# Kernel tuning notes

Hardware: AMD Instinct MI355X
Metric: run time of the kernel (lower is better)

Reference implementation:

```python
import jax, jax.numpy as jnp
import numpy as np

PATCH = 14   # vision_config.patch_size
MERGE = 2    # spatial_merge_size
D = 1024     # vision_config.hidden_size
# pixel (H, W) per image; all dims divisible by PATCH*MERGE = 28
IMAGE_SIZES = np.array([[1540, 1232], [1120, 1540], [896, 1260],
                        [1540, 1540], [1260, 896], [728, 1540]], dtype=np.int64)


def setup_inputs() -> dict:
    key = jax.random.key(0)
    k1, k2 = jax.random.split(key)
    hs = IMAGE_SIZES[:, 0] // PATCH
    ws = IMAGE_SIZES[:, 1] // PATCH
    total_tokens = int(np.sum(hs * ws))  # 47820
    image_features = jax.random.normal(k1, (total_tokens, D), dtype=jnp.float32)
    # nn.Linear(D*MERGE**2 -> D, bias=False): weight [D, D*MERGE**2]
    weight = jax.random.normal(k2, (D, D * MERGE * MERGE), dtype=jnp.float32) * 0.02
    return {"image_features": image_features, "weight": weight,
            "image_sizes": IMAGE_SIZES}


def _merge_patches(image_features, image_sizes):
    """Per-image unfold(kernel=stride=MERGE) -> [n_blocks, D*MERGE^2], concatenated."""
    m = MERGE
    d = image_features.shape[-1]
    sizes = np.asarray(image_sizes)
    hs = sizes[:, 0] // PATCH
    ws = sizes[:, 1] // PATCH
    offsets = np.concatenate([[0], np.cumsum(hs * ws)])
    grids = []
    for i in range(sizes.shape[0]):
        h, w = int(hs[i]), int(ws[i])
        x = jax.lax.dynamic_slice_in_dim(image_features, int(offsets[i]), h * w, 0)
        # [h, w, d] -> blocks of m x m; torch unfold layout is (d, kh, kw) channel-major
        x = x.reshape(h // m, m, w // m, m, d)
        x = x.transpose(0, 2, 4, 1, 3)           # [h/m, w/m, d, m, m]
        x = x.reshape((h // m) * (w // m), d * m * m)
        grids.append(x)
    return jnp.concatenate(grids, axis=0)        # [sum(h*w)/m^2, d*m^2]


def reference(image_features, weight, image_sizes):
    merged = _merge_patches(image_features, image_sizes)
    return merged @ weight.T                     # [N_merged, D]
```

## Files before the change

kernel.cpp:

```cpp
#include <hip/hip_runtime.h>
#include <hip/hip_bf16.h>
#include <stdint.h>

#define K_DIM 4096
#define N_DIM 1024
#define M_TOT 11955

#define BM 128
#define BN 128
#define BK 64
#define NWG_M 94
#define NWG 752

__constant__ int c_wm[6]     = {44, 55, 45, 55, 32, 55};
__constant__ int c_w[6]      = {88, 110, 90, 110, 64, 110};
__constant__ int c_tokoff[6] = {0, 9680, 18480, 24240, 36340, 42100};
__constant__ int c_blkoff[6] = {0, 2420, 4620, 6060, 9085, 10525};

typedef __attribute__((ext_vector_type(8))) short bf16x8;
typedef __attribute__((ext_vector_type(4))) float f32x4;

__global__ __launch_bounds__(256) void wperm_cvt(
    const float* __restrict__ src, __hip_bfloat16* __restrict__ dst)
{
    const int n = blockIdx.x >> 1;
    const int t = (blockIdx.x & 1) * 256 + threadIdx.x;
    const float* row = src + (size_t)n * K_DIM + t * 8;
    float4 a = *(const float4*)row;
    float4 b = *(const float4*)(row + 4);
    const float va[8] = {a.x, a.y, a.z, a.w, b.x, b.y, b.z, b.w};
    __hip_bfloat16* drow = dst + (size_t)n * K_DIM + 2 * t;
#pragma unroll
    for (int seg = 0; seg < 4; ++seg) {
        __hip_bfloat162 h = __float22bfloat162_rn(
            make_float2(va[seg], va[4 + seg]));
        *(__hip_bfloat162*)(drow + seg * 1024) = h;
    }
}

__global__ __launch_bounds__(256) void gemm_fused(
    const float* __restrict__ A,
    const __hip_bfloat16* __restrict__ Wp,
    float* __restrict__ C)
{
    __shared__ __align__(16) __hip_bfloat16 lA[BM * BK];
    __shared__ __align__(16) __hip_bfloat16 lB[BN * BK];

    const int f    = blockIdx.x;
    const int xcd  = f & 7;
    const int slot = f >> 3;
    const int gidx = xcd * NWG_M + slot;
    const int mt   = gidx >> 3;
    const int nt   = gidx & 7;
    const int m0 = mt * BM;
    const int n0 = nt * BN;

    const int tid  = threadIdx.x;
    const int lane = tid & 63;
    const int wave = tid >> 6;
    const int wm = (wave >> 1) * 64;
    const int wn = (wave & 1) * 64;
    const int al = lane & 15;
    const int q  = lane >> 4;
    const int al7 = al & 7;

    int t00[4], ww[4];
    const __hip_bfloat16* pBbase[4];
#pragma unroll
    for (int j = 0; j < 4; ++j) {
        const int c = tid + j * 256;
        const int row = c >> 3;
        const int g = (c & 7) ^ (row & 7);
        int gm = m0 + row; if (gm > M_TOT - 1) gm = M_TOT - 1;
        int img = 0;
#pragma unroll
        for (int u = 1; u < 6; ++u) if (gm >= c_blkoff[u]) img = u;
        const int bi = gm - c_blkoff[img];
        const int wmrg = c_wm[img];
        const int gi = bi / wmrg;
        const int gj = bi - gi * wmrg;
        const int w = c_w[img];
        t00[j] = c_tokoff[img] + 2 * gi * w + 2 * gj;
        pBbase[j] = Wp + (size_t)(n0 + row) * K_DIM + g * 8;
        ww[j] = w | (g << 16);
    }

    f32x4 acc[4][4];
#pragma unroll
    for (int i = 0; i < 4; ++i)
#pragma unroll
        for (int j = 0; j < 4; ++j)
            acc[i][j] = (f32x4){0.f, 0.f, 0.f, 0.f};

#pragma unroll
    for (int seg = 0; seg < 4; ++seg) {
        const int kh = seg >> 1, kw = seg & 1;
        const float* pA[4];
        const __hip_bfloat16* pB[4];
#pragma unroll
        for (int j = 0; j < 4; ++j) {
            const int w = ww[j] & 0xffff;
            const int g = ww[j] >> 16;
            pA[j] = A + (size_t)(t00[j] + kh * w + kw) * N_DIM + g * 8;
            pB[j] = pBbase[j] + seg * 1024;
        }
        for (int k2 = 0; k2 < 1024; k2 += BK) {
#pragma unroll
            for (int j = 0; j < 4; ++j)
                __builtin_amdgcn_global_load_lds(
                    (const __attribute__((address_space(1))) void*)(pB[j] + k2),
                    (__attribute__((address_space(3))) void*)(lB + (tid + j * 256) * 8),
                    16, 0, 0);
            float4 ra[4][2];
#pragma unroll
            for (int j = 0; j < 4; ++j) {
                const float4* s = (const float4*)(pA[j] + k2);
                ra[j][0] = s[0];
                ra[j][1] = s[1];
            }
#pragma unroll
            for (int j = 0; j < 4; ++j) {
                union { __hip_bfloat162 h2[4]; uint4 u; } pk;
                pk.h2[0] = __float22bfloat162_rn(make_float2(ra[j][0].x, ra[j][0].y));
                pk.h2[1] = __float22bfloat162_rn(make_float2(ra[j][0].z, ra[j][0].w));
                pk.h2[2] = __float22bfloat162_rn(make_float2(ra[j][1].x, ra[j][1].y));
                pk.h2[3] = __float22bfloat162_rn(make_float2(ra[j][1].z, ra[j][1].w));
                *(uint4*)(lA + (size_t)(tid + j * 256) * 8) = pk.u;
            }
            __syncthreads();

            bf16x8 af[4], bfr[4];
#pragma unroll
            for (int ks = 0; ks < 2; ++ks) {
#pragma unroll
                for (int mi = 0; mi < 4; ++mi) {
                    const int r = wm + mi * 16 + al;
                    const int p = (ks * 4 + q) ^ al7;
                    af[mi] = *(const bf16x8*)(lA + r * BK + p * 8);
                }
#pragma unroll
                for (int ni = 0; ni < 4; ++ni) {
                    const int r = wn + ni * 16 + al;
                    const int p = (ks * 4 + q) ^ al7;
                    bfr[ni] = *(const bf16x8*)(lB + r * BK + p * 8);
                }
#pragma unroll
                for (int mi = 0; mi < 4; ++mi)
#pragma unroll
                    for (int ni = 0; ni < 4; ++ni)
                        acc[mi][ni] = __builtin_amdgcn_mfma_f32_16x16x32_bf16(
                            af[mi], bfr[ni], acc[mi][ni], 0, 0, 0);
            }
            __syncthreads();
        }
    }

#pragma unroll
    for (int mi = 0; mi < 4; ++mi) {
        const int row = m0 + wm + mi * 16 + q * 4;
#pragma unroll
        for (int ni = 0; ni < 4; ++ni) {
            const int col = n0 + wn + ni * 16 + al;
            float* cp = C + (size_t)row * N_DIM + col;
#pragma unroll
            for (int rg = 0; rg < 4; ++rg) {
                if (row + rg < M_TOT) cp[(size_t)rg * N_DIM] = acc[mi][ni][rg];
            }
        }
    }
}

extern "C" void kernel_launch(void* const* d_in, const int* in_sizes, int n_in,
                              void* d_out, int out_size, void* d_ws, size_t ws_size,
                              hipStream_t stream)
{
    const float* feat = (const float*)d_in[0];
    const float* wgt  = (const float*)d_in[1];
    float* out = (float*)d_out;

    __hip_bfloat16* wp = (__hip_bfloat16*)d_ws;

    wperm_cvt<<<2048, 256, 0, stream>>>(wgt, wp);
    gemm_fused<<<NWG, 256, 0, stream>>>(feat, wp, out);
}
```

Measured before the change: 463.9 us.

## Double-buffer LDS tiles to overlap next-tile global loads with MFMA compute

Result: slower. 499.8 us (+7.7%).

```diff
diff --git a/kernel.cpp b/kernel.cpp
--- a/kernel.cpp
+++ b/kernel.cpp
@@ -11,6 +11,7 @@
 #define BK 64
 #define NWG_M 94
 #define NWG 752
+#define KT_TOT 64
 
 __constant__ int c_wm[6]     = {44, 55, 45, 55, 32, 55};
 __constant__ int c_w[6]      = {88, 110, 90, 110, 64, 110};
@@ -43,8 +44,8 @@
     const __hip_bfloat16* __restrict__ Wp,
     float* __restrict__ C)
 {
-    __shared__ __align__(16) __hip_bfloat16 lA[BM * BK];
-    __shared__ __align__(16) __hip_bfloat16 lB[BN * BK];
+    __shared__ __align__(16) __hip_bfloat16 lA[2][BM * BK];
+    __shared__ __align__(16) __hip_bfloat16 lB[2][BN * BK];
 
     const int f    = blockIdx.x;
     const int xcd  = f & 7;
@@ -64,7 +65,7 @@
     const int q  = lane >> 4;
     const int al7 = al & 7;
 
-    int t00[4], ww[4];
+    int t00[4], wwA[4];
     const __hip_bfloat16* pBbase[4];
 #pragma unroll
     for (int j = 0; j < 4; ++j) {
@@ -82,7 +83,46 @@
         const int w = c_w[img];
         t00[j] = c_tokoff[img] + 2 * gi * w + 2 * gj;
         pBbase[j] = Wp + (size_t)(n0 + row) * K_DIM + g * 8;
-        ww[j] = w | (g << 16);
+        wwA[j] = w | (g << 16);
+    }
+
+    auto aptr = [&](int j, int kt) -> const float* {
+        const int seg = kt >> 4;
+        const int k2  = (kt & 15) * BK;
+        const int kh = seg >> 1, kw = seg & 1;
+        const int w = wwA[j] & 0xffff;
+        const int g = wwA[j] >> 16;
+        return A + (size_t)(t00[j] + (kh ? w : 0) + kw) * N_DIM + g * 8 + k2;
+    };
+    auto bptr = [&](int j, int kt) -> const __hip_bfloat16* {
+        const int seg = kt >> 4;
+        const int k2  = (kt & 15) * BK;
+        return pBbase[j] + seg * 1024 + k2;
+    };
+
+    {
+        float4 ra[4][2];
+#pragma unroll
+        for (int j = 0; j < 4; ++j) {
+            const float4* s = (const float4*)aptr(j, 0);
+            ra[j][0] = s[0]; ra[j][1] = s[1];
+        }
+#pragma unroll
+        for (int j = 0; j < 4; ++j)
+            __builtin_amdgcn_global_load_lds(
+                (const __attribute__((address_space(1))) void*)bptr(j, 0),
+                (__attribute__((address_space(3))) void*)(&lB[0][0] + (tid + j * 256) * 8),
+                16, 0, 0);
+#pragma unroll
+        for (int j = 0; j < 4; ++j) {
+            union { __hip_bfloat162 h2[4]; uint4 u; } pk;
+            pk.h2[0] = __float22bfloat162_rn(make_float2(ra[j][0].x, ra[j][0].y));
+            pk.h2[1] = __float22bfloat162_rn(make_float2(ra[j][0].z, ra[j][0].w));
+            pk.h2[2] = __float22bfloat162_rn(make_float2(ra[j][1].x, ra[j][1].y));
+            pk.h2[3] = __float22bfloat162_rn(make_float2(ra[j][1].z, ra[j][1].w));
+            *(uint4*)(&lA[0][0] + (tid + j * 256) * 8) = pk.u;
+        }
+        __syncthreads();
     }
 
     f32x4 acc[4][4];
@@ -92,32 +132,52 @@
         for (int j = 0; j < 4; ++j)
             acc[i][j] = (f32x4){0.f, 0.f, 0.f, 0.f};
 
-#pragma unroll
-    for (int seg = 0; seg < 4; ++seg) {
-        const int kh = seg >> 1, kw = seg & 1;
-        const float* pA[4];
-        const __hip_bfloat16* pB[4];
-#pragma unroll
-        for (int j = 0; j < 4; ++j) {
-            const int w = ww[j] & 0xffff;
-            const int g = ww[j] >> 16;
-            pA[j] = A + (size_t)(t00[j] + kh * w + kw) * N_DIM + g * 8;
-            pB[j] = pBbase[j] + seg * 1024;
-        }
-        for (int k2 = 0; k2 < 1024; k2 += BK) {
+    for (int kt = 0; kt < KT_TOT; ++kt) {
+        const int cur = kt & 1;
+        const int nxt = cur ^ 1;
+        const bool more = (kt + 1 < KT_TOT);
+
+        float4 ra[4][2];
+        if (more) {
+#pragma unroll
+            for (int j = 0; j < 4; ++j) {
+                const float4* s = (const float4*)aptr(j, kt + 1);
+                ra[j][0] = s[0]; ra[j][1] = s[1];
+            }
 #pragma unroll
             for (int j = 0; j < 4; ++j)
                 __builtin_amdgcn_global_load_lds(
-                    (const __attribute__((address_space(1))) void*)(pB[j] + k2),
-                    (__attribute__((address_space(3))) void*)(lB + (tid + j * 256) * 8),
+                    (const __attribute__((address_space(1))) void*)bptr(j, kt + 1),
+                    (__attribute__((address_space(3))) void*)(&lB[nxt][0] + (tid + j * 256) * 8),
                     16, 0, 0);
-            float4 ra[4][2];
-#pragma unroll
-            for (int j = 0; j < 4; ++j) {
-                const float4* s = (const float4*)(pA[j] + k2);
-                ra[j][0] = s[0];
-                ra[j][1] = s[1];
-            }
+        }
+
+        const __hip_bfloat16* la = &lA[cur][0];
+        const __hip_bfloat16* lb = &lB[cur][0];
+        bf16x8 af[4], bfr[4];
+#pragma unroll
+        for (int ks = 0; ks < 2; ++ks) {
+#pragma unroll
+            for (int mi = 0; mi < 4; ++mi) {
+                const int r = wm + mi * 16 + al;
+                const int p = (ks * 4 + q) ^ al7;
+                af[mi] = *(const bf16x8*)(la + r * BK + p * 8);
+            }
+#pragma unroll
+            for (int ni = 0; ni < 4; ++ni) {
+                const int r = wn + ni * 16 + al;
+                const int p = (ks * 4 + q) ^ al7;
+                bfr[ni] = *(const bf16x8*)(lb + r * BK + p * 8);
+            }
+#pragma unroll
+            for (int mi = 0; mi < 4; ++mi)
+#pragma unroll
+                for (int ni = 0; ni < 4; ++ni)
+                    acc[mi][ni] = __builtin_amdgcn_mfma_f32_16x16x32_bf16(
+                        af[mi], bfr[ni], acc[mi][ni], 0, 0, 0);
+        }
+
+        if (more) {
 #pragma unroll
             for (int j = 0; j < 4; ++j) {
                 union { __hip_bfloat162 h2[4]; uint4 u; } pk;
@@ -125,34 +185,10 @@
                 pk.h2[1] = __float22bfloat162_rn(make_float2(ra[j][0].z, ra[j][0].w));
                 pk.h2[2] = __float22bfloat162_rn(make_float2(ra[j][1].x, ra[j][1].y));
                 pk.h2[3] = __float22bfloat162_rn(make_float2(ra[j][1].z, ra[j][1].w));
-                *(uint4*)(lA + (size_t)(tid + j * 256) * 8) = pk.u;
-            }
-            __syncthreads();
-
-            bf16x8 af[4], bfr[4];
-#pragma unroll
-            for (int ks = 0; ks < 2; ++ks) {
-#pragma unroll
-                for (int mi = 0; mi < 4; ++mi) {
-                    const int r = wm + mi * 16 + al;
-                    const int p = (ks * 4 + q) ^ al7;
-                    af[mi] = *(const bf16x8*)(lA + r * BK + p * 8);
-                }
-#pragma unroll
-                for (int ni = 0; ni < 4; ++ni) {
-                    const int r = wn + ni * 16 + al;
-                    const int p = (ks * 4 + q) ^ al7;
-                    bfr[ni] = *(const bf16x8*)(lB + r * BK + p * 8);
-                }
-#pragma unroll
-                for (int mi = 0; mi < 4; ++mi)
-#pragma unroll
-                    for (int ni = 0; ni < 4; ++ni)
-                        acc[mi][ni] = __builtin_amdgcn_mfma_f32_16x16x32_bf16(
-                            af[mi], bfr[ni], acc[mi][ni], 0, 0, 0);
-            }
-            __syncthreads();
-        }
+                *(uint4*)(&lA[nxt][0] + (tid + j * 256) * 8) = pk.u;
+            }
+        }
+        __syncthreads();
     }
 
 #pragma unroll
```

## Pre-unfold activations to bf16 and use double-buffered 256x256 GEMM tiles

Applied to the files above, without the earlier changes.

Result: faster. 448.6 us (-3.3%).

```diff
diff --git a/kernel.cpp b/kernel.cpp
--- a/kernel.cpp
+++ b/kernel.cpp
@@ -6,11 +6,13 @@
 #define N_DIM 1024
 #define M_TOT 11955
 
-#define BM 128
-#define BN 128
+#define BM 256
+#define BN 256
 #define BK 64
-#define NWG_M 94
-#define NWG 752
+#define KT_N 64
+#define M_TILES 47
+#define N_TILES 4
+#define NWG 188
 
 __constant__ int c_wm[6]     = {44, 55, 45, 55, 32, 55};
 __constant__ int c_w[6]      = {88, 110, 90, 110, 64, 110};
@@ -19,6 +21,11 @@
 
 typedef __attribute__((ext_vector_type(8))) short bf16x8;
 typedef __attribute__((ext_vector_type(4))) float f32x4;
+
+#define BARRIER() do { asm volatile("" ::: "memory"); \
+                       __builtin_amdgcn_s_barrier();  \
+                       asm volatile("" ::: "memory"); } while (0)
+#define VMCNT0()  asm volatile("s_waitcnt vmcnt(0)" ::: "memory")
 
 __global__ __launch_bounds__(256) void wperm_cvt(
     const float* __restrict__ src, __hip_bfloat16* __restrict__ dst)
@@ -38,125 +45,164 @@
     }
 }
 
-__global__ __launch_bounds__(256) void gemm_fused(
-    const float* __restrict__ A,
+__global__ __launch_bounds__(256) void unfold_cvt(
+    const float* __restrict__ feat, __hip_bfloat16* __restrict__ Am)
+{
+    const int m = blockIdx.x;
+    const int t = threadIdx.x;
+    const int seg = t >> 6;
+    const int d0 = (t & 63) * 16;
+    int img = 0;
+#pragma unroll
+    for (int u = 1; u < 6; ++u) if (m >= c_blkoff[u]) img = u;
+    const int bi = m - c_blkoff[img];
+    const int wmrg = c_wm[img];
+    const int gi = bi / wmrg;
+    const int gj = bi - gi * wmrg;
+    const int w  = c_w[img];
+    const int kh = seg >> 1, kw = seg & 1;
+    const int tok = c_tokoff[img] + 2 * gi * w + 2 * gj + kh * w + kw;
+    const float4* src = (const float4*)(feat + (size_t)tok * N_DIM + d0);
+    float4 v0 = src[0], v1 = src[1], v2 = src[2], v3 = src[3];
+    union { __hip_bfloat162 h[8]; uint4 u4[2]; } pk;
+    pk.h[0] = __float22bfloat162_rn(make_float2(v0.x, v0.y));
+    pk.h[1] = __float22bfloat162_rn(make_float2(v0.z, v0.w));
+    pk.h[2] = __float22bfloat162_rn(make_float2(v1.x, v1.y));
+    pk.h[3] = __float22bfloat162_rn(make_float2(v1.z, v1.w));
+    pk.h[4] = __float22bfloat162_rn(make_float2(v2.x, v2.y));
+    pk.h[5] = __float22bfloat162_rn(make_float2(v2.z, v2.w));
+    pk.h[6] = __float22bfloat162_rn(make_float2(v3.x, v3.y));
+    pk.h[7] = __float22bfloat162_rn(make_float2(v3.z, v3.w));
+    uint4* dst = (uint4*)(Am + (size_t)m * K_DIM + seg * 1024 + d0);
+    dst[0] = pk.u4[0];
+    dst[1] = pk.u4[1];
+}
+
+__global__ __launch_bounds__(512, 2) void gemm8(
+    const __hip_bfloat16* __restrict__ Am,
     const __hip_bfloat16* __restrict__ Wp,
     float* __restrict__ C)
 {
-    __shared__ __align__(16) __hip_bfloat16 lA[BM * BK];
-    __shared__ __align__(16) __hip_bfloat16 lB[BN * BK];
-
-    const int f    = blockIdx.x;
-    const int xcd  = f & 7;
-    const int slot = f >> 3;
-    const int gidx = xcd * NWG_M + slot;
-    const int mt   = gidx >> 3;
-    const int nt   = gidx & 7;
+    __shared__ __align__(16) __hip_bfloat16 lA[2][BM * BK];
+    __shared__ __align__(16) __hip_bfloat16 lB[2][BN * BK];
+
+    const int orig = blockIdx.x;
+    const int x    = orig & 7;
+    const int idx  = orig >> 3;
+    const int start = (x < 4) ? x * 24 : 96 + (x - 4) * 23;
+    const int wgid  = start + idx;
+    const int mt = wgid >> 2;
+    const int nt = wgid & 3;
     const int m0 = mt * BM;
     const int n0 = nt * BN;
 
     const int tid  = threadIdx.x;
     const int lane = tid & 63;
     const int wave = tid >> 6;
-    const int wm = (wave >> 1) * 64;
-    const int wn = (wave & 1) * 64;
+    const int wm = (wave >> 2) * 128;
+    const int wn = (wave & 3) * 64;
     const int al = lane & 15;
     const int q  = lane >> 4;
     const int al7 = al & 7;
 
-    int t00[4], ww[4];
-    const __hip_bfloat16* pBbase[4];
-#pragma unroll
-    for (int j = 0; j < 4; ++j) {
-        const int c = tid + j * 256;
-        const int row = c >> 3;
-        const int g = (c & 7) ^ (row & 7);
-        int gm = m0 + row; if (gm > M_TOT - 1) gm = M_TOT - 1;
-        int img = 0;
-#pragma unroll
-        for (int u = 1; u < 6; ++u) if (gm >= c_blkoff[u]) img = u;
-        const int bi = gm - c_blkoff[img];
-        const int wmrg = c_wm[img];
-        const int gi = bi / wmrg;
-        const int gj = bi - gi * wmrg;
-        const int w = c_w[img];
-        t00[j] = c_tokoff[img] + 2 * gi * w + 2 * gj;
-        pBbase[j] = Wp + (size_t)(n0 + row) * K_DIM + g * 8;
-        ww[j] = w | (g << 16);
-    }
-
-    f32x4 acc[4][4];
+    const __hip_bfloat16* srcA[4];
+    const __hip_bfloat16* srcB[4];
+#pragma unroll
+    for (int i = 0; i < 4; ++i) {
+        const int c = tid + i * 512;
+        const int r = c >> 3;
+        const int g = (c & 7) ^ (r & 7);
+        int gm = m0 + r; if (gm > M_TOT - 1) gm = M_TOT - 1;
+        srcA[i] = Am + (size_t)gm * K_DIM + g * 8;
+        srcB[i] = Wp + (size_t)(n0 + r) * K_DIM + g * 8;
+    }
+
 #pragma unroll
     for (int i = 0; i < 4; ++i)
+        __builtin_amdgcn_global_load_lds(
+            (const __attribute__((address_space(1))) void*)srcA[i],
+            (__attribute__((address_space(3))) void*)(&lA[0][0] + (tid + i * 512) * 8),
+            16, 0, 0);
+#pragma unroll
+    for (int i = 0; i < 4; ++i)
+        __builtin_amdgcn_global_load_lds(
+            (const __attribute__((address_space(1))) void*)srcB[i],
+            (__attribute__((address_space(3))) void*)(&lB[0][0] + (tid + i * 512) * 8),
+            16, 0, 0);
+    __syncthreads();
+
+    f32x4 acc[8][4];
+#pragma unroll
+    for (int i = 0; i < 8; ++i)
 #pragma unroll
         for (int j = 0; j < 4; ++j)
             acc[i][j] = (f32x4){0.f, 0.f, 0.f, 0.f};
 
-#pragma unroll
-    for (int seg = 0; seg < 4; ++seg) {
-        const int kh = seg >> 1, kw = seg & 1;
-        const float* pA[4];
-        const __hip_bfloat16* pB[4];
-#pragma unroll
-        for (int j = 0; j < 4; ++j) {
-            const int w = ww[j] & 0xffff;
-            const int g = ww[j] >> 16;
-            pA[j] = A + (size_t)(t00[j] + kh * w + kw) * N_DIM + g * 8;
-            pB[j] = pBbase[j] + seg * 1024;
+    for (int kt = 0; kt < KT_N; ++kt) {
+        const int cur = kt & 1;
+        const __hip_bfloat16* la = &lA[cur][0];
+        const __hip_bfloat16* lb = &lB[cur][0];
+        __hip_bfloat16* wa = &lA[cur ^ 1][0];
+        __hip_bfloat16* wb = &lB[cur ^ 1][0];
+        const bool more = (kt + 1 < KT_N);
+        const int koff = (kt + 1) * BK;
+
+        bf16x8 bfr[4][2];
+#pragma unroll
+        for (int p = 0; p < 4; ++p) {
+            if (p == 0) {
+#pragma unroll
+                for (int ks = 0; ks < 2; ++ks)
+#pragma unroll
+                    for (int ni = 0; ni < 4; ++ni) {
+                        const int r = wn + ni * 16 + al;
+                        bfr[ni][ks] = *(const bf16x8*)(
+                            lb + r * BK + (((ks * 4 + q) ^ al7) * 8));
+                    }
+            }
+            bf16x8 af[2][2];
+#pragma unroll
+            for (int ks = 0; ks < 2; ++ks)
+#pragma unroll
+                for (int mm = 0; mm < 2; ++mm) {
+                    const int r = wm + (p * 2 + mm) * 16 + al;
+                    af[mm][ks] = *(const bf16x8*)(
+                        la + r * BK + (((ks * 4 + q) ^ al7) * 8));
+                }
+            if (p == 0 && more) {
+#pragma unroll
+                for (int i = 0; i < 4; ++i)
+                    __builtin_amdgcn_global_load_lds(
+                        (const __attribute__((address_space(1))) void*)(srcA[i] + koff),
+                        (__attribute__((address_space(3))) void*)(wa + (tid + i * 512) * 8),
+                        16, 0, 0);
+            }
+            if (p == 1 && more) {
+#pragma unroll
+                for (int i = 0; i < 4; ++i)
+                    __builtin_amdgcn_global_load_lds(
+                        (const __attribute__((address_space(1))) void*)(srcB[i] + koff),
+                        (__attribute__((address_space(3))) void*)(wb + (tid + i * 512) * 8),
+                        16, 0, 0);
+            }
+            BARRIER();
+            __builtin_amdgcn_s_setprio(1);
+#pragma unroll
+            for (int ks = 0; ks < 2; ++ks)
+#pragma unroll
+                for (int mm = 0; mm < 2; ++mm)
+#pragma unroll
+                    for (int ni = 0; ni < 4; ++ni)
+                        acc[p * 2 + mm][ni] = __builtin_amdgcn_mfma_f32_16x16x32_bf16(
+                            af[mm][ks], bfr[ni][ks], acc[p * 2 + mm][ni], 0, 0, 0);
+            __builtin_amdgcn_s_setprio(0);
+            if (p == 3) VMCNT0();
+            BARRIER();
         }
-        for (int k2 = 0; k2 < 1024; k2 += BK) {
-#pragma unroll
-            for (int j = 0; j < 4; ++j)
-                __builtin_amdgcn_global_load_lds(
-                    (const __attribute__((address_space(1))) void*)(pB[j] + k2),
-                    (__attribute__((address_space(3))) void*)(lB + (tid + j * 256) * 8),
-                    16, 0, 0);
-            float4 ra[4][2];
-#pragma unroll
-            for (int j = 0; j < 4; ++j) {
-                const float4* s = (const float4*)(pA[j] + k2);
-                ra[j][0] = s[0];
-                ra[j][1] = s[1];
-            }
-#pragma unroll
-            for (int j = 0; j < 4; ++j) {
-                union { __hip_bfloat162 h2[4]; uint4 u; } pk;
-                pk.h2[0] = __float22bfloat162_rn(make_float2(ra[j][0].x, ra[j][0].y));
-                pk.h2[1] = __float22bfloat162_rn(make_float2(ra[j][0].z, ra[j][0].w));
-                pk.h2[2] = __float22bfloat162_rn(make_float2(ra[j][1].x, ra[j][1].y));
-                pk.h2[3] = __float22bfloat162_rn(make_float2(ra[j][1].z, ra[j][1].w));
-                *(uint4*)(lA + (size_t)(tid + j * 256) * 8) = pk.u;
-            }
-            __syncthreads();
-
-            bf16x8 af[4], bfr[4];
-#pragma unroll
-            for (int ks = 0; ks < 2; ++ks) {
-#pragma unroll
-                for (int mi = 0; mi < 4; ++mi) {
-                    const int r = wm + mi * 16 + al;
-                    const int p = (ks * 4 + q) ^ al7;
-                    af[mi] = *(const bf16x8*)(lA + r * BK + p * 8);
-                }
-#pragma unroll
-                for (int ni = 0; ni < 4; ++ni) {
-                    const int r = wn + ni * 16 + al;
-                    const int p = (ks * 4 + q) ^ al7;
-                    bfr[ni] = *(const bf16x8*)(lB + r * BK + p * 8);
-                }
-#pragma unroll
-                for (int mi = 0; mi < 4; ++mi)
-#pragma unroll
-                    for (int ni = 0; ni < 4; ++ni)
-                        acc[mi][ni] = __builtin_amdgcn_mfma_f32_16x16x32_bf16(
-                            af[mi], bfr[ni], acc[mi][ni], 0, 0, 0);
-            }
-            __syncthreads();
-        }
-    }
-
-#pragma unroll
-    for (int mi = 0; mi < 4; ++mi) {
+    }
+
+#pragma unroll
+    for (int mi = 0; mi < 8; ++mi) {
         const int row = m0 + wm + mi * 16 + q * 4;
 #pragma unroll
         for (int ni = 0; ni < 4; ++ni) {
@@ -178,8 +224,11 @@
     const float* wgt  = (const float*)d_in[1];
     float* out = (float*)d_out;
 
-    __hip_bfloat16* wp = (__hip_bfloat16*)d_ws;
+    __hip_bfloat16* Am = (__hip_bfloat16*)d_ws;
+    __hip_bfloat16* wp = (__hip_bfloat16*)((char*)d_ws +
+                         (size_t)M_TOT * K_DIM * sizeof(__hip_bfloat16));
 
     wperm_cvt<<<2048, 256, 0, stream>>>(wgt, wp);
-    gemm_fused<<<NWG, 256, 0, stream>>>(feat, wp, out);
-}
+    unfold_cvt<<<M_TOT, 256, 0, stream>>>(feat, Am);
+    gemm8<<<NWG, 512, 0, stream>>>(Am, wp, out);
+}
```

## Split unfold and bf16 conversion into separate pass before GEMM

Applied to the files above, without the earlier changes.

After: 471.0 us. No clear change (+1.5%).

```diff
diff --git a/kernel.cpp b/kernel.cpp
--- a/kernel.cpp
+++ b/kernel.cpp
@@ -38,8 +38,41 @@
     }
 }
 
-__global__ __launch_bounds__(256) void gemm_fused(
-    const float* __restrict__ A,
+__global__ __launch_bounds__(256) void unfold_cvt(
+    const float* __restrict__ feat, __hip_bfloat16* __restrict__ Am)
+{
+    const int m = blockIdx.x;
+    const int t = threadIdx.x;
+    const int seg = t >> 6;
+    const int d0 = (t & 63) * 16;
+    int img = 0;
+#pragma unroll
+    for (int u = 1; u < 6; ++u) if (m >= c_blkoff[u]) img = u;
+    const int bi = m - c_blkoff[img];
+    const int wmrg = c_wm[img];
+    const int gi = bi / wmrg;
+    const int gj = bi - gi * wmrg;
+    const int w  = c_w[img];
+    const int kh = seg >> 1, kw = seg & 1;
+    const int tok = c_tokoff[img] + 2 * gi * w + 2 * gj + kh * w + kw;
+    const float4* src = (const float4*)(feat + (size_t)tok * N_DIM + d0);
+    float4 v0 = src[0], v1 = src[1], v2 = src[2], v3 = src[3];
+    union { __hip_bfloat162 h[8]; uint4 u4[2]; } pk;
+    pk.h[0] = __float22bfloat162_rn(make_float2(v0.x, v0.y));
+    pk.h[1] = __float22bfloat162_rn(make_float2(v0.z, v0.w));
+    pk.h[2] = __float22bfloat162_rn(make_float2(v1.x, v1.y));
+    pk.h[3] = __float22bfloat162_rn(make_float2(v1.z, v1.w));
+    pk.h[4] = __float22bfloat162_rn(make_float2(v2.x, v2.y));
+    pk.h[5] = __float22bfloat162_rn(make_float2(v2.z, v2.w));
+    pk.h[6] = __float22bfloat162_rn(make_float2(v3.x, v3.y));
+    pk.h[7] = __float22bfloat162_rn(make_float2(v3.z, v3.w));
+    uint4* dst = (uint4*)(Am + (size_t)m * K_DIM + seg * 1024 + d0);
+    dst[0] = pk.u4[0];
+    dst[1] = pk.u4[1];
+}
+
+__global__ __launch_bounds__(256) void gemm_bt(
+    const __hip_bfloat16* __restrict__ Am,
     const __hip_bfloat16* __restrict__ Wp,
     float* __restrict__ C)
 {
@@ -49,9 +82,9 @@
     const int f    = blockIdx.x;
     const int xcd  = f & 7;
     const int slot = f >> 3;
-    const int gidx = xcd * NWG_M + slot;
-    const int mt   = gidx >> 3;
-    const int nt   = gidx & 7;
+    const int wgid = xcd * NWG_M + slot;
+    const int mt   = wgid >> 3;
+    const int nt   = wgid & 7;
     const int m0 = mt * BM;
     const int n0 = nt * BN;
 
@@ -64,25 +97,16 @@
     const int q  = lane >> 4;
     const int al7 = al & 7;
 
-    int t00[4], ww[4];
-    const __hip_bfloat16* pBbase[4];
+    const __hip_bfloat16* srcA[4];
+    const __hip_bfloat16* srcB[4];
 #pragma unroll
     for (int j = 0; j < 4; ++j) {
         const int c = tid + j * 256;
         const int row = c >> 3;
         const int g = (c & 7) ^ (row & 7);
         int gm = m0 + row; if (gm > M_TOT - 1) gm = M_TOT - 1;
-        int img = 0;
-#pragma unroll
-        for (int u = 1; u < 6; ++u) if (gm >= c_blkoff[u]) img = u;
-        const int bi = gm - c_blkoff[img];
-        const int wmrg = c_wm[img];
-        const int gi = bi / wmrg;
-        const int gj = bi - gi * wmrg;
-        const int w = c_w[img];
-        t00[j] = c_tokoff[img] + 2 * gi * w + 2 * gj;
-        pBbase[j] = Wp + (size_t)(n0 + row) * K_DIM + g * 8;
-        ww[j] = w | (g << 16);
+        srcA[j] = Am + (size_t)gm * K_DIM + g * 8;
+        srcB[j] = Wp + (size_t)(n0 + row) * K_DIM + g * 8;
     }
 
     f32x4 acc[4][4];
@@ -92,67 +116,44 @@
         for (int j = 0; j < 4; ++j)
             acc[i][j] = (f32x4){0.f, 0.f, 0.f, 0.f};
 
+    for (int k2 = 0; k2 < K_DIM; k2 += BK) {
 #pragma unroll
-    for (int seg = 0; seg < 4; ++seg) {
-        const int kh = seg >> 1, kw = seg & 1;
-        const float* pA[4];
-        const __hip_bfloat16* pB[4];
+        for (int j = 0; j < 4; ++j)
+            __builtin_amdgcn_global_load_lds(
+                (const __attribute__((address_space(1))) void*)(srcA[j] + k2),
+                (__attribute__((address_space(3))) void*)(lA + (tid + j * 256) * 8),
+                16, 0, 0);
 #pragma unroll
-        for (int j = 0; j < 4; ++j) {
-            const int w = ww[j] & 0xffff;
-            const int g = ww[j] >> 16;
-            pA[j] = A + (size_t)(t00[j] + kh * w + kw) * N_DIM + g * 8;
-            pB[j] = pBbase[j] + seg * 1024;
-        }
-        for (int k2 = 0; k2 < 1024; k2 += BK) {
+        for (int j = 0; j < 4; ++j)
+            __builtin_amdgcn_global_load_lds(
+                (const __attribute__((address_space(1))) void*)(srcB[j] + k2),
+                (__attribute__((address_space(3))) void*)(lB + (tid + j * 256) * 8),
+                16, 0, 0);
+        __syncthreads();
+
+        bf16x8 af[4], bfr[4];
 #pragma unroll
-            for (int j = 0; j < 4; ++j)
-                __builtin_amdgcn_global_load_lds(
-                    (const __attribute__((address_space(1))) void*)(pB[j] + k2),
-                    (__attribute__((address_space(3))) void*)(lB + (tid + j * 256) * 8),
-                    16, 0, 0);
-            float4 ra[4][2];
+        for (int ks = 0; ks < 2; ++ks) {
 #pragma unroll
-            for (int j = 0; j < 4; ++j) {
-                const float4* s = (const float4*)(pA[j] + k2);
-                ra[j][0] = s[0];
-                ra[j][1] = s[1];
+            for (int mi = 0; mi < 4; ++mi) {
+                const int r = wm + mi * 16 + al;
+                const int p = (ks * 4 + q) ^ al7;
+                af[mi] = *(const bf16x8*)(lA + r * BK + p * 8);
             }
 #pragma unroll
-            for (int j = 0; j < 4; ++j) {
-                union { __hip_bfloat162 h2[4]; uint4 u; } pk;
-                pk.h2[0] = __float22bfloat162_rn(make_float2(ra[j][0].x, ra[j][0].y));
-                pk.h2[1] = __float22bfloat162_rn(make_float2(ra[j][0].z, ra[j][0].w));
-                pk.h2[2] = __float22bfloat162_rn(make_float2(ra[j][1].x, ra[j][1].y));
-                pk.h2[3] = __float22bfloat162_rn(make_float2(ra[j][1].z, ra[j][1].w));
-                *(uint4*)(lA + (size_t)(tid + j * 256) * 8) = pk.u;
+            for (int ni = 0; ni < 4; ++ni) {
+                const int r = wn + ni * 16 + al;
+                const int p = (ks * 4 + q) ^ al7;
+                bfr[ni] = *(const bf16x8*)(lB + r * BK + p * 8);
             }
-            __syncthreads();
-
-            bf16x8 af[4], bfr[4];
 #pragma unroll
-            for (int ks = 0; ks < 2; ++ks) {
+            for (int mi = 0; mi < 4; ++mi)
 #pragma unroll
-                for (int mi = 0; mi < 4; ++mi) {
-                    const int r = wm + mi * 16 + al;
-                    const int p = (ks * 4 + q) ^ al7;
-                    af[mi] = *(const bf16x8*)(lA + r * BK + p * 8);
-                }
-#pragma unroll
-                for (int ni = 0; ni < 4; ++ni) {
-                    const int r = wn + ni * 16 + al;
-                    const int p = (ks * 4 + q) ^ al7;
-                    bfr[ni] = *(const bf16x8*)(lB + r * BK + p * 8);
-                }
-#pragma unroll
-                for (int mi = 0; mi < 4; ++mi)
-#pragma unroll
-                    for (int ni = 0; ni < 4; ++ni)
-                        acc[mi][ni] = __builtin_amdgcn_mfma_f32_16x16x32_bf16(
-                            af[mi], bfr[ni], acc[mi][ni], 0, 0, 0);
-            }
-            __syncthreads();
+                for (int ni = 0; ni < 4; ++ni)
+                    acc[mi][ni] = __builtin_amdgcn_mfma_f32_16x16x32_bf16(
+                        af[mi], bfr[ni], acc[mi][ni], 0, 0, 0);
         }
+        __syncthreads();
     }
 
 #pragma unroll
@@ -178,8 +179,11 @@
     const float* wgt  = (const float*)d_in[1];
     float* out = (float*)d_out;
 
-    __hip_bfloat16* wp = (__hip_bfloat16*)d_ws;
+    __hip_bfloat16* Am = (__hip_bfloat16*)d_ws;
+    __hip_bfloat16* wp = (__hip_bfloat16*)((char*)d_ws +
+                         (size_t)M_TOT * K_DIM * sizeof(__hip_bfloat16));
 
     wperm_cvt<<<2048, 256, 0, stream>>>(wgt, wp);
-    gemm_fused<<<NWG, 256, 0, stream>>>(feat, wp, out);
+    unfold_cvt<<<M_TOT, 256, 0, stream>>>(feat, Am);
+    gemm_bt<<<NWG, 256, 0, stream>>>(Am, wp, out);
 }
```
